# Performance work log

Hardware: AMD Instinct MI355X
Metric: run time of the kernel (lower is better)

## Reference

```python
import jax, jax.numpy as jnp
import numpy as np

# BERT-base geometry
B, N, H, DH = 4, 512, 12, 64
HID = H * DH            # 768
E = 65536               # total edges (~avg degree 32)
NREL = 64               # relation vocabulary


def setup_inputs() -> dict:
    key = jax.random.key(0)
    ks = jax.random.split(key, 12)
    node_states = jax.random.normal(ks[0], (B, N, HID), jnp.float32)
    b = jax.random.randint(ks[1], (E,), 0, B)
    hn = jax.random.randint(ks[2], (E,), 0, N)
    tn = jax.random.randint(ks[3], (E,), 0, N)
    r = jax.random.randint(ks[4], (E,), 0, NREL)
    edge_indices = jnp.stack([b, hn, tn, r]).astype(jnp.int32)  # (4, E)
    node_type_ids = jnp.zeros((B, N), jnp.int32)  # unused by this subclass
    sc = 0.02
    Wq = jax.random.normal(ks[5], (HID, HID), jnp.float32) * sc
    bq = jnp.zeros((HID,), jnp.float32)
    Wk = jax.random.normal(ks[6], (HID, HID), jnp.float32) * sc
    bk = jnp.zeros((HID,), jnp.float32)
    Wv = jax.random.normal(ks[7], (HID, HID), jnp.float32) * sc
    bv = jnp.zeros((HID,), jnp.float32)
    # relation matrix embeddings: one (DH, DH) matrix per relation id
    rel_emb = jnp.eye(DH, dtype=jnp.float32)[None] + jax.random.normal(ks[8], (NREL, DH, DH), jnp.float32) * sc
    return {"node_states": node_states, "edge_indices": edge_indices,
            "node_type_ids": node_type_ids, "Wq": Wq, "bq": bq,
            "Wk": Wk, "bk": bk, "Wv": Wv, "bv": bv, "rel_emb": rel_emb}


def reference(node_states, edge_indices, node_type_ids, Wq, bq, Wk, bk, Wv, bv, rel_emb):
    Bq, Nn, hid = node_states.shape
    # dense QKV projections (torch Linear: y = x @ W^T + b)
    Q = node_states @ Wq.T + bq
    K = node_states @ Wk.T + bk
    V = (node_states @ Wv.T + bv).reshape(Bq, Nn, H, DH)  # (B,N,H,D)
    be, he, te, re = edge_indices  # each (E,)
    # per-edge gathers
    Qe = Q[be, he].reshape(-1, H, DH)   # (E,H,D)
    Ke = K[be, te].reshape(-1, H, DH)   # (E,H,D)
    Re = rel_emb[re]                     # (E,D,D) relation matrix per edge
    # Q projected through relation matrix, then inner product with K per head
    Qp = jnp.einsum('ehd,edk->ehk', Qe, Re)
    logits = jnp.einsum('ehd,ehd->eh', Qp, Ke) / jnp.sqrt(jnp.float32(DH))  # (E,H)
    # sparse softmax over tail nodes: segment = (batch, head_node)
    seg = be * Nn + he
    nseg = Bq * Nn
    m = jax.ops.segment_max(logits, seg, num_segments=nseg)      # (BN,H)
    ex = jnp.exp(logits - m[seg])
    denom = jax.ops.segment_sum(ex, seg, num_segments=nseg)      # (BN,H)
    p = ex / denom[seg]                                          # (E,H)
    # dropout prob = 0.0 (deterministic reference)
    # aggregate: out[b,i,h,:] = sum_edges p_e * V[b, tail_e, h, :]
    contrib = p[:, :, None] * V[be, te]                          # (E,H,D)
    out = jax.ops.segment_sum(contrib, seg, num_segments=nseg)   # (BN,H,D)
    return out.reshape(Bq, Nn, H * DH)
```

## Files before the change

### kernel.cpp

```cpp
#include <hip/hip_runtime.h>
#include <hip/hip_bf16.h>

#define NB   4
#define NN   512
#define NH   12
#define DHD  64
#define HID  768
#define NE   65536
#define NSEG 2048
#define NREL 64
#define NSUB 32
#define NRSUB (NREL * NSUB)
#define LGS  16
#define POISON 0xAAAAAAAAu

typedef short bf16x8 __attribute__((ext_vector_type(8)));
typedef float f32x4  __attribute__((ext_vector_type(4)));
typedef unsigned short u16x8 __attribute__((ext_vector_type(8)));

__device__ __forceinline__ unsigned short f2bf(float f) {
    __hip_bfloat16 h = __float2bfloat16(f);
    return *reinterpret_cast<unsigned short*>(&h);
}
__device__ __forceinline__ float bf2f(unsigned short s) {
    return __int_as_float(((int)s) << 16);
}
__device__ __forceinline__ int unpz(int v) {
    return (int)((unsigned)v - POISON);
}
__device__ __forceinline__ void load_lds16(const void* g, void* l) {
    __builtin_amdgcn_global_load_lds(
        (const __attribute__((address_space(1))) unsigned int*)g,
        (__attribute__((address_space(3))) unsigned int*)l, 16, 0, 0);
}

#define NX4 ((2048 * 768) / 4)
#define NW4 ((768 * 768) / 4)
#define NCAST ((NX4 + 3 * NW4) / 256)
__global__ __launch_bounds__(256) void cast_hist_kernel(
    const float* __restrict__ X, const float* __restrict__ Wq,
    const float* __restrict__ Wk, const float* __restrict__ Wv,
    unsigned short* __restrict__ Xh, unsigned short* __restrict__ Wh,
    const int* __restrict__ ei,
    int* __restrict__ count, int* __restrict__ rcount2)
{
    if (blockIdx.x >= NCAST) {
        const int e = (blockIdx.x - NCAST) * 256 + threadIdx.x;
        const int b  = ei[e];
        const int hn = ei[NE + e];
        const int rr = ei[3 * NE + e];
        const int sub = (e >> 8) & (NSUB - 1);
        atomicAdd(&count[b * NN + hn], 1);
        atomicAdd(&rcount2[rr * NSUB + sub], 1);
        return;
    }
    const int i = blockIdx.x * 256 + threadIdx.x;
    float4 v;
    ushort4* dst;
    if (i < NX4) {
        v = ((const float4*)X)[i];
        dst = &((ushort4*)Xh)[i];
    } else {
        const int j = i - NX4;
        const float* W = (j < NW4) ? Wq : ((j < 2 * NW4) ? Wk : Wv);
        const int jj = (j < NW4) ? j : ((j < 2 * NW4) ? j - NW4 : j - 2 * NW4);
        v = ((const float4*)W)[jj];
        dst = &((ushort4*)Wh)[j];
    }
    ushort4 r;
    r.x = f2bf(v.x); r.y = f2bf(v.y); r.z = f2bf(v.z); r.w = f2bf(v.w);
    *dst = r;
}

#define NQKV 576
__global__ __launch_bounds__(256) void qkv_scatter_kernel(
    const unsigned short* __restrict__ Xh, const unsigned short* __restrict__ Wh,
    const float* __restrict__ bq, const float* __restrict__ bk,
    const float* __restrict__ bv,
    unsigned short* __restrict__ Qh, unsigned short* __restrict__ Kh,
    unsigned short* __restrict__ Vh,
    const int* __restrict__ ei,
    const int* __restrict__ count, const int* __restrict__ rcount2,
    int* __restrict__ cursor, int* __restrict__ rcursor2,
    int* __restrict__ s_te, int* __restrict__ s_pk, int* __restrict__ r_pos,
    int* __restrict__ offs_g, int* __restrict__ rofs2_g)
{
    __shared__ __align__(16) char smem[64 * 132 * 4];
    const int tid = threadIdx.x;

    if (blockIdx.x >= NQKV) {
        int* offs_l = (int*)smem;
        int* rofs_l = offs_l + NSEG;
        int* buf    = rofs_l + NRSUB;
        int* extra  = buf + 256;

        {
            int local[8];
            int s = 0;
            #pragma unroll
            for (int i = 0; i < 8; ++i) { local[i] = unpz(count[tid * 8 + i]); s += local[i]; }
            buf[tid] = s;
            __syncthreads();
            for (int off = 1; off < 256; off <<= 1) {
                const int v = (tid >= off) ? buf[tid - off] : 0;
                __syncthreads();
                buf[tid] += v;
                __syncthreads();
            }
            int run = buf[tid] - s;
            #pragma unroll
            for (int i = 0; i < 8; ++i) { offs_l[tid * 8 + i] = run; run += local[i]; }
            if (tid == 255) extra[0] = run;
            __syncthreads();
        }
        {
            int local[8];
            int s = 0;
            #pragma unroll
            for (int i = 0; i < 8; ++i) { local[i] = unpz(rcount2[tid * 8 + i]); s += local[i]; }
            buf[tid] = s;
            __syncthreads();
            for (int off = 1; off < 256; off <<= 1) {
                const int v = (tid >= off) ? buf[tid - off] : 0;
                __syncthreads();
                buf[tid] += v;
                __syncthreads();
            }
            int run = buf[tid] - s;
            #pragma unroll
            for (int i = 0; i < 8; ++i) { rofs_l[tid * 8 + i] = run; run += local[i]; }
            if (blockIdx.x == NQKV && tid == 255) rofs2_g[NRSUB] = run;
        }
        __syncthreads();

        if (blockIdx.x == NQKV) {
            #pragma unroll
            for (int i = 0; i < 8; ++i) {
                offs_g[tid * 8 + i]  = offs_l[tid * 8 + i];
                rofs2_g[tid * 8 + i] = rofs_l[tid * 8 + i];
            }
            if (tid == 255) offs_g[NSEG] = extra[0];
        }

        const int e = (blockIdx.x - NQKV) * 256 + tid;
        const int b  = ei[e];
        const int hn = ei[NE + e];
        const int tn = ei[2 * NE + e];
        const int rr = ei[3 * NE + e];
        const int sub = (e >> 8) & (NSUB - 1);
        const int seg = b * NN + hn;
        const int pos = offs_l[seg] + unpz(atomicAdd(&cursor[seg], 1));
        s_te[pos] = tn;
        s_pk[pos] = (seg << 9) | tn;
        const int rb = rr * NSUB + sub;
        const int rj = unpz(atomicAdd(&rcursor2[rb], 1));
        r_pos[rofs_l[rb] + rj] = pos;
        return;
    }

    const int bid = blockIdx.x;
    const int z   = bid / 192;
    const int rem = bid - z * 192;
    const int by  = rem / 6;
    const int bx  = rem - by * 6;
    const unsigned short* W = Wh + (size_t)z * (768 * 768);
    const float* bias = (z == 0) ? bq : ((z == 1) ? bk : bv);

    const int n0 = bx * 128;
    const int m0 = by * 64;
    const int lane = tid & 63;
    const int wave = tid >> 6;
    const int wm = wave >> 1, wn = wave & 1;

    unsigned short* As = (unsigned short*)smem;
    unsigned short* Bs = (unsigned short*)(smem + 8192);
    float* Cs = (float*)smem;

    f32x4 acc[2][4];
    #pragma unroll
    for (int a = 0; a < 2; ++a)
        #pragma unroll
        for (int b2 = 0; b2 < 4; ++b2) acc[a][b2] = (f32x4){0.f, 0.f, 0.f, 0.f};

    const int ml = lane & 15;
    const int q4 = lane >> 4;

    for (int k0 = 0; k0 < HID; k0 += 64) {
        __syncthreads();
        #pragma unroll
        for (int i = 0; i < 2; ++i) {
            const int slotb = i * 256 + wave * 64;
            const int idx = slotb + lane;
            const int row = idx >> 3;
            const int kq  = (idx & 7) ^ (row & 7);
            load_lds16(Xh + (size_t)(m0 + row) * HID + k0 + kq * 8,
                       As + slotb * 8);
        }
        #pragma unroll
        for (int i = 0; i < 4; ++i) {
            const int slotb = i * 256 + wave * 64;
            const int idx = slotb + lane;
            const int row = idx >> 3;
            const int kq  = (idx & 7) ^ (row & 7);
            load_lds16(W + (size_t)(n0 + row) * HID + k0 + kq * 8,
                       Bs + slotb * 8);
        }
        __syncthreads();

        #pragma unroll
        for (int ks = 0; ks < 2; ++ks) {
            bf16x8 af[2], bfr[4];
            #pragma unroll
            for (int t = 0; t < 2; ++t) {
                const int ar = wm * 32 + t * 16 + ml;
                const int ac = (ks * 4 + q4) ^ (ar & 7);
                af[t] = *(const bf16x8*)(As + ar * 64 + ac * 8);
            }
            #pragma unroll
            for (int t = 0; t < 4; ++t) {
                const int br = wn * 64 + t * 16 + ml;
                const int bc = (ks * 4 + q4) ^ (br & 7);
                bfr[t] = *(const bf16x8*)(Bs + br * 64 + bc * 8);
            }
            #pragma unroll
            for (int mt = 0; mt < 2; ++mt)
                #pragma unroll
                for (int nt = 0; nt < 4; ++nt)
                    acc[mt][nt] = __builtin_amdgcn_mfma_f32_16x16x32_bf16(
                        af[mt], bfr[nt], acc[mt][nt], 0, 0, 0);
        }
    }

    __syncthreads();
    #pragma unroll
    for (int mt = 0; mt < 2; ++mt)
        #pragma unroll
        for (int nt = 0; nt < 4; ++nt)
            #pragma unroll
            for (int rg = 0; rg < 4; ++rg)
                Cs[(wm * 32 + mt * 16 + q4 * 4 + rg) * 132 +
                   wn * 64 + nt * 16 + ml] = acc[mt][nt][rg];
    __syncthreads();

    unsigned short* Y = (z == 0) ? Qh : ((z == 1) ? Kh : Vh);
    #pragma unroll
    for (int it = 0; it < 4; ++it) {
        const int id  = tid + it * 256;
        const int row = id >> 4;
        const int cg  = id & 15;
        const float* cp = Cs + row * 132 + cg * 8;
        const float4 cA = *(const float4*)cp;
        const float4 cB = *(const float4*)(cp + 4);
        const float* bp = bias + n0 + cg * 8;
        const float4 bA = *(const float4*)bp;
        const float4 bB = *(const float4*)(bp + 4);
        const size_t o = (size_t)(m0 + row) * HID + n0 + cg * 8;
        u16x8 r;
        r[0] = f2bf(cA.x + bA.x); r[1] = f2bf(cA.y + bA.y);
        r[2] = f2bf(cA.z + bA.z); r[3] = f2bf(cA.w + bA.w);
        r[4] = f2bf(cB.x + bB.x); r[5] = f2bf(cB.y + bB.y);
        r[6] = f2bf(cB.z + bB.z); r[7] = f2bf(cB.w + bB.w);
        *(u16x8*)&Y[o] = r;
    }
}

#define RLY 32
__global__ __launch_bounds__(256) void rel_logits(
    const unsigned short* __restrict__ Qh, const unsigned short* __restrict__ Kh,
    const float* __restrict__ rel,
    const int* __restrict__ rofs2, const int* __restrict__ r_pos,
    const int* __restrict__ s_pk,
    float* __restrict__ Lg)
{
    const int r = blockIdx.x;
    const int rstart = rofs2[r * NSUB];
    const int rows = (rofs2[(r + 1) * NSUB] - rstart) * NH;
    if ((int)blockIdx.y * 256 >= rows) return;
    const int tid = threadIdx.x;
    const int lane = tid & 63;
    const int wave = tid >> 6;

    __shared__ int qb[256], kb[256], oi[256];
    __shared__ float QpS[4][16][68];

    bf16x8 bfrag[2][4];
    {
        const float* Rg = rel + (size_t)r * 4096;
        const int q4 = lane >> 4, n = lane & 15;
        #pragma unroll
        for (int ks = 0; ks < 2; ++ks)
            #pragma unroll
            for (int nt = 0; nt < 4; ++nt) {
                bf16x8 f;
                #pragma unroll
                for (int j = 0; j < 8; ++j)
                    f[j] = (short)f2bf(Rg[(ks * 32 + q4 * 8 + j) * 64 + nt * 16 + n]);
                bfrag[ks][nt] = f;
            }
    }

    for (int t0 = blockIdx.y * 256; t0 < rows; t0 += RLY * 256) {
        __syncthreads();
        {
            const int rowid = t0 + tid;
            if (rowid < rows) {
                const int el = rowid / 12;
                const int h  = rowid - el * 12;
                const int pos = r_pos[rstart + el];
                const int pk  = s_pk[pos];
                const int seg = pk >> 9;
                const int te  = pk & (NN - 1);
                qb[tid] = seg * HID + h * 64;
                kb[tid] = ((seg & ~(NN - 1)) + te) * HID + h * 64;
                oi[tid] = pos * LGS + h;
            } else { qb[tid] = 0; kb[tid] = 0; oi[tid] = -1; }
        }
        __syncthreads();

        for (int g = wave; g < 16; g += 4) {
            const int m = lane & 15, q4 = lane >> 4;
            const int qbase = qb[g * 16 + m];
            f32x4 cfr[4] = {{0,0,0,0},{0,0,0,0},{0,0,0,0},{0,0,0,0}};
            #pragma unroll
            for (int ks = 0; ks < 2; ++ks) {
                const bf16x8 afr = *(const bf16x8*)(Qh + qbase + ks * 32 + q4 * 8);
                #pragma unroll
                for (int nt = 0; nt < 4; ++nt)
                    cfr[nt] = __builtin_amdgcn_mfma_f32_16x16x32_bf16(
                        afr, bfrag[ks][nt], cfr[nt], 0, 0, 0);
            }
            #pragma unroll
            for (int nt = 0; nt < 4; ++nt)
                #pragma unroll
                for (int rg = 0; rg < 4; ++rg)
                    QpS[wave][q4 * 4 + rg][nt * 16 + m] = cfr[nt][rg];

            const int rw = lane >> 2, ch = (lane & 3) * 16;
            const int rowid2 = g * 16 + rw;
            const int kbase = kb[rowid2];
            const bf16x8 k0 = *(const bf16x8*)(Kh + kbase + ch);
            const bf16x8 k1 = *(const bf16x8*)(Kh + kbase + ch + 8);
            float s = 0.f;
            #pragma unroll
            for (int i = 0; i < 8; ++i) {
                s = fmaf(QpS[wave][rw][ch + i],     bf2f((unsigned short)k0[i]), s);
                s = fmaf(QpS[wave][rw][ch + 8 + i], bf2f((unsigned short)k1[i]), s);
            }
            s += __shfl_xor(s, 1, 64);
            s += __shfl_xor(s, 2, 64);
            if ((lane & 3) == 0) {
                const int o = oi[rowid2];
                if (o >= 0) Lg[o] = __expf(s * 0.125f);
            }
        }
    }
}

__global__ __launch_bounds__(256) void seg_softmax_agg(
    const unsigned short* __restrict__ Vh, const float* __restrict__ Lg,
    const int* __restrict__ offs, const int* __restrict__ s_te,
    float* __restrict__ out)
{
    const int seg  = blockIdx.x;
    const int tid  = threadIdx.x;
    const int lane = tid & 63;
    const int w    = tid >> 6;
    const int start = offs[seg];
    const int cnt   = offs[seg + 1] - start;
    const int browbase = seg & ~(NN - 1);

    __shared__ int   te_s[64];
    __shared__ float pv[4][3][64];

    float l0 = 0.f, l1 = 0.f, l2 = 0.f;
    float acc0 = 0.f, acc1 = 0.f, acc2 = 0.f;

    for (int c0 = 0; c0 < cnt; c0 += 64) {
        const int cc = min(64, cnt - c0);
        __syncthreads();
        if (tid < cc) te_s[tid] = s_te[start + c0 + tid];
        __syncthreads();

        float p0 = 0.f, p1 = 0.f, p2 = 0.f;
        if (lane < cc) {
            const float* Lp = Lg + (size_t)(start + c0 + lane) * LGS;
            p0 = Lp[w]; p1 = Lp[4 + w]; p2 = Lp[8 + w];
        }
        float s0 = p0, s1 = p1, s2 = p2;
        #pragma unroll
        for (int o = 1; o < 64; o <<= 1) {
            s0 += __shfl_xor(s0, o, 64);
            s1 += __shfl_xor(s1, o, 64);
            s2 += __shfl_xor(s2, o, 64);
        }
        l0 += s0; l1 += s1; l2 += s2;
        pv[w][0][lane] = p0; pv[w][1][lane] = p1; pv[w][2][lane] = p2;

        for (int j = 0; j < cc; ++j) {
            const unsigned short* __restrict__ Vr =
                Vh + (size_t)(browbase + te_s[j]) * HID + lane;
            acc0 = fmaf(pv[w][0][j], bf2f(Vr[w * 64]),       acc0);
            acc1 = fmaf(pv[w][1][j], bf2f(Vr[(4 + w) * 64]), acc1);
            acc2 = fmaf(pv[w][2][j], bf2f(Vr[(8 + w) * 64]), acc2);
        }
    }

    float* Yo = out + (size_t)seg * HID;
    Yo[tid]       = (l0 > 0.f) ? acc0 / l0 : 0.f;
    Yo[tid + 256] = (l1 > 0.f) ? acc1 / l1 : 0.f;
    Yo[tid + 512] = (l2 > 0.f) ? acc2 / l2 : 0.f;
}

extern "C" void kernel_launch(void* const* d_in, const int* in_sizes, int n_in,
                              void* d_out, int out_size, void* d_ws, size_t ws_size,
                              hipStream_t stream)
{
    const float* X   = (const float*)d_in[0];
    const int*   EI  = (const int*)d_in[1];
    const float* Wq  = (const float*)d_in[3];
    const float* bq  = (const float*)d_in[4];
    const float* Wk  = (const float*)d_in[5];
    const float* bk  = (const float*)d_in[6];
    const float* Wv  = (const float*)d_in[7];
    const float* bv  = (const float*)d_in[8];
    const float* rel = (const float*)d_in[9];
    float* out = (float*)d_out;

    char* p = (char*)d_ws;
    unsigned short* Qh = (unsigned short*)p;  p += (size_t)NSEG * HID * 2;
    unsigned short* Kh = (unsigned short*)p;  p += (size_t)NSEG * HID * 2;
    unsigned short* Vh = (unsigned short*)p;  p += (size_t)NSEG * HID * 2;
    unsigned short* Xh = (unsigned short*)p;
    float* Lg = (float*)p;                    p += (size_t)NE * LGS * 4;
    unsigned short* Wh = (unsigned short*)p;  p += (size_t)3 * 768 * 768 * 2;
    int* offs     = (int*)p;                  p += 2052 * 4;
    int* rofs2    = (int*)p;                  p += (NRSUB + 4) * 4;
    int* count    = (int*)p;                  p += NSEG * 4;
    int* cursor   = (int*)p;                  p += NSEG * 4;
    int* rcount2  = (int*)p;                  p += NRSUB * 4;
    int* rcursor2 = (int*)p;                  p += NRSUB * 4;
    int* s_te     = (int*)p;                  p += NE * 4;
    int* s_pk     = (int*)p;                  p += NE * 4;
    int* r_pos    = (int*)p;                  p += NE * 4;

    cast_hist_kernel<<<NCAST + 256, 256, 0, stream>>>(
        X, Wq, Wk, Wv, Xh, Wh, EI, count, rcount2);
    qkv_scatter_kernel<<<NQKV + 256, 256, 0, stream>>>(
        Xh, Wh, bq, bk, bv, Qh, Kh, Vh,
        EI, count, rcount2, cursor, rcursor2, s_te, s_pk, r_pos, offs, rofs2);
    rel_logits<<<dim3(NREL, RLY), 256, 0, stream>>>(Qh, Kh, rel, rofs2, r_pos,
                                                    s_pk, Lg);
    seg_softmax_agg<<<NSEG, 256, 0, stream>>>(Vh, Lg, offs, s_te, out);
}
```

Baseline: 159.0 us.

## Pre-swizzle relation matrices to bf16 fragments and pack edge indices into int2

Adds blocks to the cast kernel that convert each relation matrix to bf16 and lay it out in MFMA fragment order once, so rel_logits loads each fragment with one vector load instead of 8 strided fp32 loads and conversions. The separate s_pk and r_pos arrays become one int2 array holding the packed index and position, which removes a dependent gather in rel_logits. The grid y dimension of rel_logits grows from 32 to 48. The softmax kernel now rewrites the poison values into the counters for the next call and clamps indices with masks, which adds a little work and couples correctness across launches.

```diff
diff --git a/kernel.cpp b/kernel.cpp
--- a/kernel.cpp
+++ b/kernel.cpp
@@ -12,6 +12,7 @@
 #define NSUB 32
 #define NRSUB (NREL * NSUB)
 #define LGS  16
+#define RLY  48
 #define POISON 0xAAAAAAAAu
 
 typedef short bf16x8 __attribute__((ext_vector_type(8)));
@@ -40,10 +41,32 @@
 __global__ __launch_bounds__(256) void cast_hist_kernel(
     const float* __restrict__ X, const float* __restrict__ Wq,
     const float* __restrict__ Wk, const float* __restrict__ Wv,
+    const float* __restrict__ rel,
     unsigned short* __restrict__ Xh, unsigned short* __restrict__ Wh,
+    unsigned short* __restrict__ Rh,
     const int* __restrict__ ei,
     int* __restrict__ count, int* __restrict__ rcount2)
 {
+    if (blockIdx.x >= NCAST + 256) {
+        __shared__ __align__(16) unsigned short fr[4096];
+        const int r = blockIdx.x - (NCAST + 256);
+        const float* Rg = rel + (size_t)r * 4096;
+        const int tid = threadIdx.x;
+        #pragma unroll
+        for (int it = 0; it < 16; ++it) {
+            const int i = it * 256 + tid;
+            const int d = i >> 6, c = i & 63;
+            const int ks = d >> 5, q4 = (d >> 3) & 3, j = d & 7;
+            const int nt = c >> 4, n = c & 15;
+            fr[((ks * 4 + nt) * 64 + q4 * 16 + n) * 8 + j] = f2bf(Rg[i]);
+        }
+        __syncthreads();
+        #pragma unroll
+        for (int v = 0; v < 2; ++v)
+            *(u16x8*)(Rh + (size_t)r * 4096 + (tid * 2 + v) * 8) =
+                *(const u16x8*)(fr + (tid * 2 + v) * 8);
+        return;
+    }
     if (blockIdx.x >= NCAST) {
         const int e = (blockIdx.x - NCAST) * 256 + threadIdx.x;
         const int b  = ei[e];
@@ -82,7 +105,7 @@
     const int* __restrict__ ei,
     const int* __restrict__ count, const int* __restrict__ rcount2,
     int* __restrict__ cursor, int* __restrict__ rcursor2,
-    int* __restrict__ s_te, int* __restrict__ s_pk, int* __restrict__ r_pos,
+    int* __restrict__ s_te, int* __restrict__ s_pkr,
     int* __restrict__ offs_g, int* __restrict__ rofs2_g)
 {
     __shared__ __align__(16) char smem[64 * 132 * 4];
@@ -149,12 +172,13 @@
         const int rr = ei[3 * NE + e];
         const int sub = (e >> 8) & (NSUB - 1);
         const int seg = b * NN + hn;
-        const int pos = offs_l[seg] + unpz(atomicAdd(&cursor[seg], 1));
+        const int pos = (offs_l[seg] + unpz(atomicAdd(&cursor[seg], 1))) & (NE - 1);
         s_te[pos] = tn;
-        s_pk[pos] = (seg << 9) | tn;
         const int rb = rr * NSUB + sub;
         const int rj = unpz(atomicAdd(&rcursor2[rb], 1));
-        r_pos[rofs_l[rb] + rj] = pos;
+        const int rslot = (rofs_l[rb] + rj) & (NE - 1);
+        int2 pv2; pv2.x = (seg << 9) | tn; pv2.y = pos;
+        ((int2*)s_pkr)[rslot] = pv2;
         return;
     }
 
@@ -264,17 +288,18 @@
     }
 }
 
-#define RLY 32
 __global__ __launch_bounds__(256) void rel_logits(
     const unsigned short* __restrict__ Qh, const unsigned short* __restrict__ Kh,
-    const float* __restrict__ rel,
-    const int* __restrict__ rofs2, const int* __restrict__ r_pos,
-    const int* __restrict__ s_pk,
+    const unsigned short* __restrict__ Rh,
+    const int* __restrict__ rofs2, const int* __restrict__ s_pkr,
     float* __restrict__ Lg)
 {
     const int r = blockIdx.x;
-    const int rstart = rofs2[r * NSUB];
-    const int rows = (rofs2[(r + 1) * NSUB] - rstart) * NH;
+    int rstart = rofs2[r * NSUB];
+    int rend   = rofs2[(r + 1) * NSUB];
+    rstart = (rstart < 0) ? 0 : ((rstart > NE) ? NE : rstart);
+    rend   = (rend < rstart) ? rstart : ((rend > NE) ? NE : rend);
+    const int rows = (rend - rstart) * NH;
     if ((int)blockIdx.y * 256 >= rows) return;
     const int tid = threadIdx.x;
     const int lane = tid & 63;
@@ -285,18 +310,12 @@
 
     bf16x8 bfrag[2][4];
     {
-        const float* Rg = rel + (size_t)r * 4096;
-        const int q4 = lane >> 4, n = lane & 15;
+        const unsigned short* Rb = Rh + (size_t)r * 4096;
         #pragma unroll
         for (int ks = 0; ks < 2; ++ks)
             #pragma unroll
-            for (int nt = 0; nt < 4; ++nt) {
-                bf16x8 f;
-                #pragma unroll
-                for (int j = 0; j < 8; ++j)
-                    f[j] = (short)f2bf(Rg[(ks * 32 + q4 * 8 + j) * 64 + nt * 16 + n]);
-                bfrag[ks][nt] = f;
-            }
+            for (int nt = 0; nt < 4; ++nt)
+                bfrag[ks][nt] = *(const bf16x8*)(Rb + ((ks * 4 + nt) * 64 + lane) * 8);
     }
 
     for (int t0 = blockIdx.y * 256; t0 < rows; t0 += RLY * 256) {
@@ -306,12 +325,13 @@
             if (rowid < rows) {
                 const int el = rowid / 12;
                 const int h  = rowid - el * 12;
-                const int pos = r_pos[rstart + el];
-                const int pk  = s_pk[pos];
-                const int seg = pk >> 9;
+                const int2 v = ((const int2*)s_pkr)[rstart + el];
+                const int pk  = v.x;
+                const int pos = v.y & (NE - 1);
+                const int sg  = (pk >> 9) & (NSEG - 1);
                 const int te  = pk & (NN - 1);
-                qb[tid] = seg * HID + h * 64;
-                kb[tid] = ((seg & ~(NN - 1)) + te) * HID + h * 64;
+                qb[tid] = sg * HID + h * 64;
+                kb[tid] = ((sg & ~(NN - 1)) + te) * HID + h * 64;
                 oi[tid] = pos * LGS + h;
             } else { qb[tid] = 0; kb[tid] = 0; oi[tid] = -1; }
         }
@@ -359,14 +379,23 @@
 __global__ __launch_bounds__(256) void seg_softmax_agg(
     const unsigned short* __restrict__ Vh, const float* __restrict__ Lg,
     const int* __restrict__ offs, const int* __restrict__ s_te,
-    float* __restrict__ out)
+    float* __restrict__ out,
+    int* __restrict__ count, int* __restrict__ cursor,
+    int* __restrict__ rcount2, int* __restrict__ rcursor2)
 {
     const int seg  = blockIdx.x;
     const int tid  = threadIdx.x;
+    if (tid < 4) {
+        int* cp = (tid == 0) ? count : ((tid == 1) ? cursor
+                 : ((tid == 2) ? rcount2 : rcursor2));
+        cp[seg] = (int)POISON;
+    }
     const int lane = tid & 63;
     const int w    = tid >> 6;
-    const int start = offs[seg];
-    const int cnt   = offs[seg + 1] - start;
+    int start = offs[seg];
+    int cnt   = offs[seg + 1] - start;
+    start &= (NE - 1);
+    cnt = (cnt > NE) ? NE : cnt;
     const int browbase = seg & ~(NN - 1);
 
     __shared__ int   te_s[64];
@@ -378,12 +407,12 @@
     for (int c0 = 0; c0 < cnt; c0 += 64) {
         const int cc = min(64, cnt - c0);
         __syncthreads();
-        if (tid < cc) te_s[tid] = s_te[start + c0 + tid];
+        if (tid < cc) te_s[tid] = s_te[(start + c0 + tid) & (NE - 1)] & (NN - 1);
         __syncthreads();
 
         float p0 = 0.f, p1 = 0.f, p2 = 0.f;
         if (lane < cc) {
-            const float* Lp = Lg + (size_t)(start + c0 + lane) * LGS;
+            const float* Lp = Lg + (size_t)((start + c0 + lane) & (NE - 1)) * LGS;
             p0 = Lp[w]; p1 = Lp[4 + w]; p2 = Lp[8 + w];
         }
         float s0 = p0, s1 = p1, s2 = p2;
@@ -433,6 +462,7 @@
     unsigned short* Xh = (unsigned short*)p;
     float* Lg = (float*)p;                    p += (size_t)NE * LGS * 4;
     unsigned short* Wh = (unsigned short*)p;  p += (size_t)3 * 768 * 768 * 2;
+    unsigned short* Rh = (unsigned short*)p;  p += (size_t)NREL * 4096 * 2;
     int* offs     = (int*)p;                  p += 2052 * 4;
     int* rofs2    = (int*)p;                  p += (NRSUB + 4) * 4;
     int* count    = (int*)p;                  p += NSEG * 4;
@@ -440,15 +470,14 @@
     int* rcount2  = (int*)p;                  p += NRSUB * 4;
     int* rcursor2 = (int*)p;                  p += NRSUB * 4;
     int* s_te     = (int*)p;                  p += NE * 4;
-    int* s_pk     = (int*)p;                  p += NE * 4;
-    int* r_pos    = (int*)p;                  p += NE * 4;
-
-    cast_hist_kernel<<<NCAST + 256, 256, 0, stream>>>(
-        X, Wq, Wk, Wv, Xh, Wh, EI, count, rcount2);
+    int* s_pkr    = (int*)p;                  p += (size_t)NE * 8;
+
+    cast_hist_kernel<<<NCAST + 256 + NREL, 256, 0, stream>>>(
+        X, Wq, Wk, Wv, rel, Xh, Wh, Rh, EI, count, rcount2);
     qkv_scatter_kernel<<<NQKV + 256, 256, 0, stream>>>(
         Xh, Wh, bq, bk, bv, Qh, Kh, Vh,
-        EI, count, rcount2, cursor, rcursor2, s_te, s_pk, r_pos, offs, rofs2);
-    rel_logits<<<dim3(NREL, RLY), 256, 0, stream>>>(Qh, Kh, rel, rofs2, r_pos,
-                                                    s_pk, Lg);
-    seg_softmax_agg<<<NSEG, 256, 0, stream>>>(Vh, Lg, offs, s_te, out);
-}
+        EI, count, rcount2, cursor, rcursor2, s_te, s_pkr, offs, rofs2);
+    rel_logits<<<dim3(NREL, RLY), 256, 0, stream>>>(Qh, Kh, Rh, rofs2, s_pkr, Lg);
+    seg_softmax_agg<<<NSEG, 256, 0, stream>>>(Vh, Lg, offs, s_te, out,
+                                              count, cursor, rcount2, rcursor2);
+}
```

Result: no change. 161.5 us (+1.5%).

## Replace histogram and prefix-scan with fixed-capacity buckets and fuse bf16 cast into GEMM

Applied to the files above, without the earlier changes.

Drops the separate cast and histogram kernel. The QKV GEMM now converts fp32 X and W to bf16 while staging tiles into LDS. Edges are scattered into fixed-capacity slots: 128 per segment and 256 per relation sub-bucket, addressed straight from atomic cursors, so no prefix scan is needed. The aggregation kernel resets the cursors to the poison value for the next call. This removes one launch and a serial scan, but it loses the async global-to-LDS loads and silently overwrites or drops edges if any bucket exceeds its capacity.

```diff
diff --git a/kernel.cpp b/kernel.cpp
--- a/kernel.cpp
+++ b/kernel.cpp
@@ -9,9 +9,12 @@
 #define NE   65536
 #define NSEG 2048
 #define NREL 64
-#define NSUB 32
-#define NRSUB (NREL * NSUB)
 #define LGS  16
+#define SCAP 128
+#define NSUB2 8
+#define RSUB (NREL * NSUB2)
+#define RCAP 256
+#define RLY2 12
 #define POISON 0xAAAAAAAAu
 
 typedef short bf16x8 __attribute__((ext_vector_type(8)));
@@ -28,133 +31,37 @@
 __device__ __forceinline__ int unpz(int v) {
     return (int)((unsigned)v - POISON);
 }
-__device__ __forceinline__ void load_lds16(const void* g, void* l) {
-    __builtin_amdgcn_global_load_lds(
-        (const __attribute__((address_space(1))) unsigned int*)g,
-        (__attribute__((address_space(3))) unsigned int*)l, 16, 0, 0);
-}
-
-#define NX4 ((2048 * 768) / 4)
-#define NW4 ((768 * 768) / 4)
-#define NCAST ((NX4 + 3 * NW4) / 256)
-__global__ __launch_bounds__(256) void cast_hist_kernel(
-    const float* __restrict__ X, const float* __restrict__ Wq,
-    const float* __restrict__ Wk, const float* __restrict__ Wv,
-    unsigned short* __restrict__ Xh, unsigned short* __restrict__ Wh,
-    const int* __restrict__ ei,
-    int* __restrict__ count, int* __restrict__ rcount2)
-{
-    if (blockIdx.x >= NCAST) {
-        const int e = (blockIdx.x - NCAST) * 256 + threadIdx.x;
-        const int b  = ei[e];
-        const int hn = ei[NE + e];
-        const int rr = ei[3 * NE + e];
-        const int sub = (e >> 8) & (NSUB - 1);
-        atomicAdd(&count[b * NN + hn], 1);
-        atomicAdd(&rcount2[rr * NSUB + sub], 1);
-        return;
-    }
-    const int i = blockIdx.x * 256 + threadIdx.x;
-    float4 v;
-    ushort4* dst;
-    if (i < NX4) {
-        v = ((const float4*)X)[i];
-        dst = &((ushort4*)Xh)[i];
-    } else {
-        const int j = i - NX4;
-        const float* W = (j < NW4) ? Wq : ((j < 2 * NW4) ? Wk : Wv);
-        const int jj = (j < NW4) ? j : ((j < 2 * NW4) ? j - NW4 : j - 2 * NW4);
-        v = ((const float4*)W)[jj];
-        dst = &((ushort4*)Wh)[j];
-    }
-    ushort4 r;
-    r.x = f2bf(v.x); r.y = f2bf(v.y); r.z = f2bf(v.z); r.w = f2bf(v.w);
-    *dst = r;
-}
 
 #define NQKV 576
 __global__ __launch_bounds__(256) void qkv_scatter_kernel(
-    const unsigned short* __restrict__ Xh, const unsigned short* __restrict__ Wh,
+    const float* __restrict__ Xf,
+    const float* __restrict__ Wq, const float* __restrict__ Wk,
+    const float* __restrict__ Wv,
     const float* __restrict__ bq, const float* __restrict__ bk,
     const float* __restrict__ bv,
     unsigned short* __restrict__ Qh, unsigned short* __restrict__ Kh,
     unsigned short* __restrict__ Vh,
     const int* __restrict__ ei,
-    const int* __restrict__ count, const int* __restrict__ rcount2,
-    int* __restrict__ cursor, int* __restrict__ rcursor2,
-    int* __restrict__ s_te, int* __restrict__ s_pk, int* __restrict__ r_pos,
-    int* __restrict__ offs_g, int* __restrict__ rofs2_g)
+    int* __restrict__ cursor, int* __restrict__ rcursor,
+    int* __restrict__ s_te, int* __restrict__ s_pkr)
 {
     __shared__ __align__(16) char smem[64 * 132 * 4];
     const int tid = threadIdx.x;
 
     if (blockIdx.x >= NQKV) {
-        int* offs_l = (int*)smem;
-        int* rofs_l = offs_l + NSEG;
-        int* buf    = rofs_l + NRSUB;
-        int* extra  = buf + 256;
-
-        {
-            int local[8];
-            int s = 0;
-            #pragma unroll
-            for (int i = 0; i < 8; ++i) { local[i] = unpz(count[tid * 8 + i]); s += local[i]; }
-            buf[tid] = s;
-            __syncthreads();
-            for (int off = 1; off < 256; off <<= 1) {
-                const int v = (tid >= off) ? buf[tid - off] : 0;
-                __syncthreads();
-                buf[tid] += v;
-                __syncthreads();
-            }
-            int run = buf[tid] - s;
-            #pragma unroll
-            for (int i = 0; i < 8; ++i) { offs_l[tid * 8 + i] = run; run += local[i]; }
-            if (tid == 255) extra[0] = run;
-            __syncthreads();
-        }
-        {
-            int local[8];
-            int s = 0;
-            #pragma unroll
-            for (int i = 0; i < 8; ++i) { local[i] = unpz(rcount2[tid * 8 + i]); s += local[i]; }
-            buf[tid] = s;
-            __syncthreads();
-            for (int off = 1; off < 256; off <<= 1) {
-                const int v = (tid >= off) ? buf[tid - off] : 0;
-                __syncthreads();
-                buf[tid] += v;
-                __syncthreads();
-            }
-            int run = buf[tid] - s;
-            #pragma unroll
-            for (int i = 0; i < 8; ++i) { rofs_l[tid * 8 + i] = run; run += local[i]; }
-            if (blockIdx.x == NQKV && tid == 255) rofs2_g[NRSUB] = run;
-        }
-        __syncthreads();
-
-        if (blockIdx.x == NQKV) {
-            #pragma unroll
-            for (int i = 0; i < 8; ++i) {
-                offs_g[tid * 8 + i]  = offs_l[tid * 8 + i];
-                rofs2_g[tid * 8 + i] = rofs_l[tid * 8 + i];
-            }
-            if (tid == 255) offs_g[NSEG] = extra[0];
-        }
-
         const int e = (blockIdx.x - NQKV) * 256 + tid;
         const int b  = ei[e];
         const int hn = ei[NE + e];
         const int tn = ei[2 * NE + e];
         const int rr = ei[3 * NE + e];
-        const int sub = (e >> 8) & (NSUB - 1);
         const int seg = b * NN + hn;
-        const int pos = offs_l[seg] + unpz(atomicAdd(&cursor[seg], 1));
+        const int slot = unpz(atomicAdd(&cursor[seg], 1)) & (SCAP - 1);
+        const int pos  = seg * SCAP + slot;
         s_te[pos] = tn;
-        s_pk[pos] = (seg << 9) | tn;
-        const int rb = rr * NSUB + sub;
-        const int rj = unpz(atomicAdd(&rcursor2[rb], 1));
-        r_pos[rofs_l[rb] + rj] = pos;
+        const int rsub = rr * NSUB2 + ((e >> 8) & (NSUB2 - 1));
+        const int rj = unpz(atomicAdd(&rcursor[rsub], 1)) & (RCAP - 1);
+        int2 pv2; pv2.x = (seg << 9) | tn; pv2.y = pos;
+        ((int2*)s_pkr)[rsub * RCAP + rj] = pv2;
         return;
     }
 
@@ -163,7 +70,7 @@
     const int rem = bid - z * 192;
     const int by  = rem / 6;
     const int bx  = rem - by * 6;
-    const unsigned short* W = Wh + (size_t)z * (768 * 768);
+    const float* Wf = (z == 0) ? Wq : ((z == 1) ? Wk : Wv);
     const float* bias = (z == 0) ? bq : ((z == 1) ? bk : bv);
 
     const int n0 = bx * 128;
@@ -189,21 +96,33 @@
         __syncthreads();
         #pragma unroll
         for (int i = 0; i < 2; ++i) {
-            const int slotb = i * 256 + wave * 64;
-            const int idx = slotb + lane;
+            const int idx = i * 256 + tid;
             const int row = idx >> 3;
             const int kq  = (idx & 7) ^ (row & 7);
-            load_lds16(Xh + (size_t)(m0 + row) * HID + k0 + kq * 8,
-                       As + slotb * 8);
+            const float* s4 = Xf + (size_t)(m0 + row) * HID + k0 + kq * 8;
+            const float4 va = ((const float4*)s4)[0];
+            const float4 vb = ((const float4*)s4)[1];
+            u16x8 r8;
+            r8[0] = f2bf(va.x); r8[1] = f2bf(va.y);
+            r8[2] = f2bf(va.z); r8[3] = f2bf(va.w);
+            r8[4] = f2bf(vb.x); r8[5] = f2bf(vb.y);
+            r8[6] = f2bf(vb.z); r8[7] = f2bf(vb.w);
+            *(u16x8*)(As + idx * 8) = r8;
         }
         #pragma unroll
         for (int i = 0; i < 4; ++i) {
-            const int slotb = i * 256 + wave * 64;
-            const int idx = slotb + lane;
+            const int idx = i * 256 + tid;
             const int row = idx >> 3;
             const int kq  = (idx & 7) ^ (row & 7);
-            load_lds16(W + (size_t)(n0 + row) * HID + k0 + kq * 8,
-                       Bs + slotb * 8);
+            const float* s4 = Wf + (size_t)(n0 + row) * HID + k0 + kq * 8;
+            const float4 va = ((const float4*)s4)[0];
+            const float4 vb = ((const float4*)s4)[1];
+            u16x8 r8;
+            r8[0] = f2bf(va.x); r8[1] = f2bf(va.y);
+            r8[2] = f2bf(va.z); r8[3] = f2bf(va.w);
+            r8[4] = f2bf(vb.x); r8[5] = f2bf(vb.y);
+            r8[6] = f2bf(vb.z); r8[7] = f2bf(vb.w);
+            *(u16x8*)(Bs + idx * 8) = r8;
         }
         __syncthreads();
 
@@ -264,18 +183,18 @@
     }
 }
 
-#define RLY 32
 __global__ __launch_bounds__(256) void rel_logits(
     const unsigned short* __restrict__ Qh, const unsigned short* __restrict__ Kh,
     const float* __restrict__ rel,
-    const int* __restrict__ rofs2, const int* __restrict__ r_pos,
-    const int* __restrict__ s_pk,
+    const int* __restrict__ rcursor, const int* __restrict__ s_pkr,
     float* __restrict__ Lg)
 {
-    const int r = blockIdx.x;
-    const int rstart = rofs2[r * NSUB];
-    const int rows = (rofs2[(r + 1) * NSUB] - rstart) * NH;
+    const int rs = blockIdx.x;
+    int cnt = unpz(rcursor[rs]);
+    cnt = (cnt < 0) ? 0 : ((cnt > RCAP) ? RCAP : cnt);
+    const int rows = cnt * NH;
     if ((int)blockIdx.y * 256 >= rows) return;
+    const int r = rs >> 3;
     const int tid = threadIdx.x;
     const int lane = tid & 63;
     const int wave = tid >> 6;
@@ -299,19 +218,19 @@
             }
     }
 
-    for (int t0 = blockIdx.y * 256; t0 < rows; t0 += RLY * 256) {
+    for (int t0 = blockIdx.y * 256; t0 < rows; t0 += RLY2 * 256) {
         __syncthreads();
         {
             const int rowid = t0 + tid;
             if (rowid < rows) {
                 const int el = rowid / 12;
                 const int h  = rowid - el * 12;
-                const int pos = r_pos[rstart + el];
-                const int pk  = s_pk[pos];
-                const int seg = pk >> 9;
-                const int te  = pk & (NN - 1);
-                qb[tid] = seg * HID + h * 64;
-                kb[tid] = ((seg & ~(NN - 1)) + te) * HID + h * 64;
+                const int2 v = ((const int2*)s_pkr)[rs * RCAP + el];
+                const int pos = v.y & (NSEG * SCAP - 1);
+                const int sg  = (v.x >> 9) & (NSEG - 1);
+                const int te  = v.x & (NN - 1);
+                qb[tid] = sg * HID + h * 64;
+                kb[tid] = ((sg & ~(NN - 1)) + te) * HID + h * 64;
                 oi[tid] = pos * LGS + h;
             } else { qb[tid] = 0; kb[tid] = 0; oi[tid] = -1; }
         }
@@ -358,15 +277,22 @@
 
 __global__ __launch_bounds__(256) void seg_softmax_agg(
     const unsigned short* __restrict__ Vh, const float* __restrict__ Lg,
-    const int* __restrict__ offs, const int* __restrict__ s_te,
-    float* __restrict__ out)
+    const int* __restrict__ s_te,
+    float* __restrict__ out,
+    int* __restrict__ cursor, int* __restrict__ rcursor)
 {
     const int seg  = blockIdx.x;
     const int tid  = threadIdx.x;
+    int cnt = unpz(cursor[seg]);
+    __syncthreads();
+    if (tid == 0) {
+        cursor[seg] = (int)POISON;
+        if (seg < RSUB) rcursor[seg] = (int)POISON;
+    }
+    cnt = (cnt < 0) ? 0 : ((cnt > SCAP) ? SCAP : cnt);
+    const int base = seg * SCAP;
     const int lane = tid & 63;
     const int w    = tid >> 6;
-    const int start = offs[seg];
-    const int cnt   = offs[seg + 1] - start;
     const int browbase = seg & ~(NN - 1);
 
     __shared__ int   te_s[64];
@@ -378,12 +304,12 @@
     for (int c0 = 0; c0 < cnt; c0 += 64) {
         const int cc = min(64, cnt - c0);
         __syncthreads();
-        if (tid < cc) te_s[tid] = s_te[start + c0 + tid];
+        if (tid < cc) te_s[tid] = s_te[base + c0 + tid] & (NN - 1);
         __syncthreads();
 
         float p0 = 0.f, p1 = 0.f, p2 = 0.f;
         if (lane < cc) {
-            const float* Lp = Lg + (size_t)(start + c0 + lane) * LGS;
+            const float* Lp = Lg + (size_t)(base + c0 + lane) * LGS;
             p0 = Lp[w]; p1 = Lp[4 + w]; p2 = Lp[8 + w];
         }
         float s0 = p0, s1 = p1, s2 = p2;
@@ -430,25 +356,17 @@
     unsigned short* Qh = (unsigned short*)p;  p += (size_t)NSEG * HID * 2;
     unsigned short* Kh = (unsigned short*)p;  p += (size_t)NSEG * HID * 2;
     unsigned short* Vh = (unsigned short*)p;  p += (size_t)NSEG * HID * 2;
-    unsigned short* Xh = (unsigned short*)p;
-    float* Lg = (float*)p;                    p += (size_t)NE * LGS * 4;
-    unsigned short* Wh = (unsigned short*)p;  p += (size_t)3 * 768 * 768 * 2;
-    int* offs     = (int*)p;                  p += 2052 * 4;
-    int* rofs2    = (int*)p;                  p += (NRSUB + 4) * 4;
-    int* count    = (int*)p;                  p += NSEG * 4;
+    float* Lg = (float*)p;                    p += (size_t)NSEG * SCAP * LGS * 4;
     int* cursor   = (int*)p;                  p += NSEG * 4;
-    int* rcount2  = (int*)p;                  p += NRSUB * 4;
-    int* rcursor2 = (int*)p;                  p += NRSUB * 4;
-    int* s_te     = (int*)p;                  p += NE * 4;
-    int* s_pk     = (int*)p;                  p += NE * 4;
-    int* r_pos    = (int*)p;                  p += NE * 4;
-
-    cast_hist_kernel<<<NCAST + 256, 256, 0, stream>>>(
-        X, Wq, Wk, Wv, Xh, Wh, EI, count, rcount2);
+    int* rcursor  = (int*)p;                  p += RSUB * 4;
+    int* s_te     = (int*)p;                  p += (size_t)NSEG * SCAP * 4;
+    int* s_pkr    = (int*)p;                  p += (size_t)RSUB * RCAP * 8;
+
     qkv_scatter_kernel<<<NQKV + 256, 256, 0, stream>>>(
-        Xh, Wh, bq, bk, bv, Qh, Kh, Vh,
-        EI, count, rcount2, cursor, rcursor2, s_te, s_pk, r_pos, offs, rofs2);
-    rel_logits<<<dim3(NREL, RLY), 256, 0, stream>>>(Qh, Kh, rel, rofs2, r_pos,
-                                                    s_pk, Lg);
-    seg_softmax_agg<<<NSEG, 256, 0, stream>>>(Vh, Lg, offs, s_te, out);
-}
+        X, Wq, Wk, Wv, bq, bk, bv, Qh, Kh, Vh,
+        EI, cursor, rcursor, s_te, s_pkr);
+    rel_logits<<<dim3(RSUB, RLY2), 256, 0, stream>>>(
+        Qh, Kh, rel, rcursor, s_pkr, Lg);
+    seg_softmax_agg<<<NSEG, 256, 0, stream>>>(
+        Vh, Lg, s_te, out, cursor, rcursor);
+}
```

Measured after the change: 187.4 us. 17.8% more time.
